# Kernel optimization log

Measured on AMD Instinct MI355X. Metric: run time of the kernel, lower is better.

Reference implementation:

```python
import jax, jax.numpy as jnp
import numpy as np

PS = 8  # window_size
LOCAL = 16  # split channels

def conv1x1(x, w, b):
    return jnp.einsum('oi,bihw->bohw', w, x) + b[None, :, None, None]

def dynamic_local(x, w1, b1, w2, b2, k):
    # x: (B, C, H, W); dynamic per-(batch,channel) depthwise conv with generated kernels
    B, C, H, W = x.shape
    pooled = x.mean((2, 3))                      # (B, C) adaptive avg pool to 1x1
    h = jax.nn.relu(pooled @ w1.T + b1)
    kern = (h @ w2.T + b2).reshape(B, C, k, k)   # per-sample depthwise kernels
    def per_batch(xb, kb):
        return jax.lax.conv_general_dilated(
            xb[None], kb[:, None], (1, 1), 'SAME',
            feature_group_count=C,
            dimension_numbers=('NCHW', 'OIHW', 'NCHW'))[0]
    return jax.vmap(per_batch)(x, kern)

def channel_layernorm(x, w, b, eps=1e-6):
    # LayerNorm over channel dim (torch module's non-channels_last path)
    u = x.mean(1, keepdims=True)
    s = ((x - u) ** 2).mean(1, keepdims=True)
    xn = (x - u) / jnp.sqrt(s + eps)
    return w[None, :, None, None] * xn + b[None, :, None, None]

def fsas(x, hid_w, hid_b, dw_w, dw_b, ln_w, ln_b, out_w, out_b):
    hidden = conv1x1(x, hid_w, hid_b)
    mid = hidden.shape[1]
    dw = jax.lax.conv_general_dilated(
        hidden, dw_w[:, None], (1, 1), 'SAME',
        feature_group_count=mid,
        dimension_numbers=('NCHW', 'OIHW', 'NCHW')) + dw_b[None, :, None, None]
    q, k, v = jnp.split(dw, 3, axis=1)
    B, C, H, W = q.shape
    def patch(t):
        # (B,C,H,W) -> (B,C,H/ps,W/ps,ps,ps)
        return t.reshape(B, C, H // PS, PS, W // PS, PS).transpose(0, 1, 2, 4, 3, 5)
    qf = jnp.fft.rfft2(patch(q))
    kf = jnp.fft.rfft2(patch(k))
    out = jnp.fft.irfft2(qf * kf, s=(PS, PS))
    out = out.transpose(0, 1, 2, 4, 3, 5).reshape(B, C, H, W)
    out = channel_layernorm(out, ln_w, ln_b)
    return conv1x1(v * out, out_w, out_b)


def setup_inputs() -> dict:
    key = jax.random.key(0)
    ks = jax.random.split(key, 12)
    s = 0.02
    return {
        'x': jax.random.normal(ks[0], (4, 64, 256, 256), jnp.float32),
        'dl1_w1': jax.random.normal(ks[1], (16, 16), jnp.float32) * s,
        'dl1_b1': jnp.zeros((16,), jnp.float32),
        'dl1_w2': jax.random.normal(ks[2], (144, 16), jnp.float32) * s,
        'dl1_b2': jnp.zeros((144,), jnp.float32),
        'dl2_w1': jax.random.normal(ks[3], (16, 16), jnp.float32) * s,
        'dl2_b1': jnp.zeros((16,), jnp.float32),
        'dl2_w2': jax.random.normal(ks[4], (400, 16), jnp.float32) * s,
        'dl2_b2': jnp.zeros((400,), jnp.float32),
        'fs_hid_w': jax.random.normal(ks[5], (144, 48), jnp.float32) * s,
        'fs_hid_b': jnp.zeros((144,), jnp.float32),
        'fs_dw_w': jax.random.normal(ks[6], (144, 3, 3), jnp.float32) * s,
        'fs_dw_b': jnp.zeros((144,), jnp.float32),
        'fs_ln_w': jnp.ones((48,), jnp.float32),
        'fs_ln_b': jnp.zeros((48,), jnp.float32),
        'fs_out_w': jax.random.normal(ks[7], (48, 48), jnp.float32) * s,
        'fs_out_b': jnp.zeros((48,), jnp.float32),
        'last_w': jax.random.normal(ks[8], (64, 64), jnp.float32) * s,
        'last_b': jnp.zeros((64,), jnp.float32),
    }


def reference(x, dl1_w1, dl1_b1, dl1_w2, dl1_b2, dl2_w1, dl2_b1, dl2_w2, dl2_b2,
              fs_hid_w, fs_hid_b, fs_dw_w, fs_dw_b, fs_ln_w, fs_ln_b,
              fs_out_w, fs_out_b, last_w, last_b):
    x1, x2 = x[:, :LOCAL], x[:, LOCAL:]
    x1 = dynamic_local(x1, dl1_w1, dl1_b1, dl1_w2, dl1_b2, 3)
    x1 = dynamic_local(x1, dl2_w1, dl2_b1, dl2_w2, dl2_b2, 5)
    x2 = fsas(x2, fs_hid_w, fs_hid_b, fs_dw_w, fs_dw_b, fs_ln_w, fs_ln_b, fs_out_w, fs_out_b)
    return conv1x1(jnp.concatenate([x1, x2], axis=1), last_w, last_b)
```

## Files before the change

### kernel.cpp

```cpp
#include <hip/hip_runtime.h>

typedef _Float16 h2 __attribute__((ext_vector_type(2)));
typedef _Float16 h4 __attribute__((ext_vector_type(4)));
typedef _Float16 h8 __attribute__((ext_vector_type(8)));
typedef float f4 __attribute__((ext_vector_type(4)));

#if defined(__has_builtin)
#if __has_builtin(__builtin_amdgcn_fdot2)
#define HAS_FDOT2 1
#endif
#endif

__device__ __forceinline__ float warpsum(float v) {
    for (int off = 32; off > 0; off >>= 1) v += __shfl_down(v, off);
    return v;
}

__device__ __forceinline__ int aswz(int p, int k) {
    return p * 72 + ((((k >> 3) ^ (p >> 3)) & 7) << 3) + (k & 7);
}
__device__ __forceinline__ int sswz(int p, int k) {
    return p * 64 + ((((k >> 3) ^ (p >> 3)) & 7) << 3) + (k & 7);
}

__global__ __launch_bounds__(256) void k_prep(const float* __restrict__ hid_w,
                                              const float* __restrict__ out_w,
                                              const float* __restrict__ last_w,
                                              _Float16* __restrict__ hwH,
                                              _Float16* __restrict__ owlwH) {
    int t = blockIdx.x * 256 + threadIdx.x;
    int stride = gridDim.x * 256;
    for (int i = t; i < 10368; i += stride) {
        int n = i / 72, k = i - n * 72;
        hwH[i] = (k < 48) ? (_Float16)hid_w[n * 48 + k] : (_Float16)0.f;
    }
    for (int i = t; i < 3456; i += stride) {
        int n = i / 72, k = i - n * 72;
        owlwH[i] = (k < 48) ? (_Float16)out_w[n * 48 + k] : (_Float16)0.f;
    }
    for (int i = t; i < 4608; i += stride) {
        int n = i / 72, k = i - n * 72;
        owlwH[3456 + i] = (k < 64) ? (_Float16)last_w[n * 64 + k] : (_Float16)0.f;
    }
}

__global__ __launch_bounds__(256) void k_pool(const float* __restrict__ x, float* __restrict__ pooled1) {
    int bid = blockIdx.x;
    int b = bid >> 4, c = bid & 15;
    const float* base = x + (size_t)(b * 64 + c) * 65536;
    float s = 0.f;
    for (int i = threadIdx.x; i < 16384; i += 256) {
        float4 v = ((const float4*)base)[i];
        s += v.x + v.y + v.z + v.w;
    }
    __shared__ float red[4];
    s = warpsum(s);
    if ((threadIdx.x & 63) == 0) red[threadIdx.x >> 6] = s;
    __syncthreads();
    if (threadIdx.x == 0) pooled1[bid] = (red[0] + red[1] + red[2] + red[3]) * (1.f / 65536.f);
}

__global__ __launch_bounds__(256) void k_kern1(const float* __restrict__ pooled1,
                                               const float* __restrict__ w1, const float* __restrict__ b1,
                                               const float* __restrict__ w2, const float* __restrict__ b2,
                                               float* __restrict__ kern1) {
    __shared__ float h[64];
    int t = threadIdx.x;
    if (t < 64) {
        int b = t >> 4, j = t & 15;
        float a = b1[j];
        for (int i = 0; i < 16; ++i) a += pooled1[b * 16 + i] * w1[j * 16 + i];
        h[t] = fmaxf(a, 0.f);
    }
    __syncthreads();
    for (int i = t; i < 576; i += 256) {
        int b = i / 144, o = i - b * 144;
        float a = b2[o];
        for (int j = 0; j < 16; ++j) a += h[b * 16 + j] * w2[o * 16 + j];
        kern1[i] = a;
    }
}

__global__ __launch_bounds__(256) void k_dw3(const float* __restrict__ x,
                                             const float* __restrict__ kern1,
                                             float* __restrict__ y1, float* __restrict__ rowsum) {
    __shared__ float tile[10][258];
    __shared__ float red[8][4];
    int bid = blockIdx.x;
    int rb = bid & 31, bc = bid >> 5;
    int b = bc >> 4, c = bc & 15;
    int row0 = rb << 3;
    int col = threadIdx.x;
    const float* xc = x + ((size_t)(b * 64 + c) << 16);
#pragma unroll
    for (int j = 0; j < 10; ++j) {
        int r = row0 - 1 + j;
        tile[j][col + 1] = ((unsigned)r < 256u) ? xc[(r << 8) + col] : 0.f;
    }
    if (col < 10) { tile[col][0] = 0.f; tile[col][257] = 0.f; }
    const float* k9 = kern1 + b * 144 + c * 9;
    float kk[9];
#pragma unroll
    for (int i = 0; i < 9; ++i) kk[i] = k9[i];
    __syncthreads();
#pragma unroll
    for (int j = 0; j < 8; ++j) {
        float acc = 0.f;
#pragma unroll
        for (int dy = 0; dy < 3; ++dy)
#pragma unroll
            for (int dx = 0; dx < 3; ++dx)
                acc += kk[dy * 3 + dx] * tile[j + dy][col + dx];
        y1[((size_t)bc << 16) + ((row0 + j) << 8) + col] = acc;
        float s = warpsum(acc);
        if ((col & 63) == 0) red[j][col >> 6] = s;
    }
    __syncthreads();
    if (col < 8) rowsum[bc * 256 + row0 + col] = red[col][0] + red[col][1] + red[col][2] + red[col][3];
}

__global__ __launch_bounds__(256) void k_kern2(const float* __restrict__ rowsum,
                                               const float* __restrict__ w1, const float* __restrict__ b1,
                                               const float* __restrict__ w2, const float* __restrict__ b2,
                                               float* __restrict__ kern2) {
    __shared__ float ps[256];
    __shared__ float p2[64];
    __shared__ float h[64];
    int t = threadIdx.x;
    {
        int pair = t >> 2, seg = t & 3;
        const float* rs = rowsum + pair * 256 + seg * 64;
        float s = 0.f;
        for (int j = 0; j < 64; ++j) s += rs[j];
        ps[t] = s;
    }
    __syncthreads();
    if (t < 64) p2[t] = (ps[t * 4] + ps[t * 4 + 1] + ps[t * 4 + 2] + ps[t * 4 + 3]) * (1.f / 65536.f);
    __syncthreads();
    if (t < 64) {
        int b = t >> 4, j = t & 15;
        float a = b1[j];
        for (int i = 0; i < 16; ++i) a += p2[b * 16 + i] * w1[j * 16 + i];
        h[t] = fmaxf(a, 0.f);
    }
    __syncthreads();
    for (int i = t; i < 1600; i += 256) {
        int b = i / 400, o = i - b * 400;
        float a = b2[o];
        for (int j = 0; j < 16; ++j) a += h[b * 16 + j] * w2[o * 16 + j];
        kern2[i] = a;
    }
}

__global__ __launch_bounds__(256) void k_dw5(const float* __restrict__ y1,
                                             const float* __restrict__ kern2,
                                             float* __restrict__ x1o) {
    __shared__ float tile[12][260];
    int bid = blockIdx.x;
    int rb = bid & 31, bc = bid >> 5;
    int b = bc >> 4, c = bc & 15;
    int row0 = rb << 3;
    int col = threadIdx.x;
    const float* yc = y1 + ((size_t)bc << 16);
#pragma unroll
    for (int j = 0; j < 12; ++j) {
        int r = row0 - 2 + j;
        tile[j][col + 2] = ((unsigned)r < 256u) ? yc[(r << 8) + col] : 0.f;
    }
    if (col < 12) { tile[col][0] = 0.f; tile[col][1] = 0.f; tile[col][258] = 0.f; tile[col][259] = 0.f; }
    const float* k25 = kern2 + b * 400 + c * 25;
    float kk[25];
#pragma unroll
    for (int i = 0; i < 25; ++i) kk[i] = k25[i];
    __syncthreads();
#pragma unroll
    for (int j = 0; j < 8; ++j) {
        float acc = 0.f;
#pragma unroll
        for (int dy = 0; dy < 5; ++dy)
#pragma unroll
            for (int dx = 0; dx < 5; ++dx)
                acc += kk[dy * 5 + dx] * tile[j + dy][col + dx];
        x1o[((size_t)bc << 16) + ((row0 + j) << 8) + col] = acc;
    }
}

__global__ __launch_bounds__(512, 4) void k_fsas(const float* __restrict__ x,
                                                 const _Float16* __restrict__ hwH, const float* __restrict__ hid_b,
                                                 const float* __restrict__ dw_w, const float* __restrict__ dw_b,
                                                 const float* __restrict__ ln_w, const float* __restrict__ ln_b,
                                                 const _Float16* __restrict__ owlwH, const float* __restrict__ out_b,
                                                 const float* __restrict__ last_b,
                                                 const float* __restrict__ x1o, float* __restrict__ out) {
    __shared__ __align__(16) _Float16 Sbig[17856];
    __shared__ __align__(16) _Float16 vbuf[3456];
    __shared__ __align__(16) _Float16 qbuf[3072];
    __shared__ __align__(16) _Float16 kbuf2[6528];
    __shared__ __align__(16) float pstat[128];

    _Float16* Abuf  = Sbig;
    _Float16* hbuf  = Sbig;
    _Float16* fbuf  = Sbig;
    float*    lnp   = (float*)(Sbig + 4608);
    _Float16* outb  = Sbig + 6656;
    _Float16* sbufA = kbuf2;

    int tid = threadIdx.x;
    int lane = tid & 63;
    int wave = __builtin_amdgcn_readfirstlane(tid >> 6);
    int bid = blockIdx.x;
    int swz = ((bid & 7) << 9) | (bid >> 3);
    int b = swz >> 10;
    int rem = swz & 1023;
    int row0 = (rem >> 5) << 3, col0 = (rem & 31) << 3;

    int l16 = lane & 15, lhi = lane >> 4;
    int mb = wave * 16 + (lhi << 2);
    bool st[4], vok[4];
#pragma unroll
    for (int r = 0; r < 4; ++r) {
        int m = mb + r;
        st[r] = (m < 120);
        int yv = m / 12, xv = m - yv * 12;
        vok[r] = st[r] && (xv < 10) &&
                 ((unsigned)(row0 - 1 + yv) < 256u) && ((unsigned)(col0 - 1 + xv) < 256u);
    }

    h8 wb0[9], wb1[9];
    float biasr[9];
#pragma unroll
    for (int nt = 0; nt < 9; ++nt) {
        const _Float16* wr = hwH + (nt * 16 + l16) * 72 + (lhi << 3);
        wb0[nt] = *(const h8*)(wr);
        wb1[nt] = *(const h8*)(wr + 32);
        biasr[nt] = hid_b[nt * 16 + l16];
    }
    float xr[8];
    int fpx = lane, fgrp = wave - 6;
    if (wave >= 6) {
        size_t gp = ((size_t)(row0 + (fpx >> 3)) << 8) + col0 + (fpx & 7);
#pragma unroll
        for (int j = 0; j < 8; ++j)
            xr[j] = x1o[((size_t)(b * 16 + fgrp * 8 + j) << 16) + gp];
    }

    if (tid < 480) {
        int k = tid / 10, y = tid - (tid / 10) * 10;
        int gy = row0 - 1 + y;
        bool rowok = (unsigned)gy < 256u;
        const float* xk = x + ((size_t)(b * 64 + 16 + k) << 16) + ((size_t)(gy & 255) << 8);
#pragma unroll
        for (int xx = 0; xx < 10; ++xx) {
            int gx = col0 - 1 + xx;
            float v = (rowok && (unsigned)gx < 256u) ? xk[gx] : 0.f;
            Abuf[aswz(y * 12 + xx, k)] = (_Float16)v;
        }
        Abuf[aswz(y * 12 + 10, k)] = (_Float16)0.f;
        Abuf[aswz(y * 12 + 11, k)] = (_Float16)0.f;
    }
    if (tid < 256) {
        int p = tid >> 1, kb = 48 + ((tid & 1) << 3);
        *(h8*)(Abuf + aswz(p, kb)) = (h8)(_Float16)0.f;
    }
    if (tid < 48) {
        int p = 120 + tid / 6, kb = (tid % 6) << 3;
        *(h8*)(Abuf + aswz(p, kb)) = (h8)(_Float16)0.f;
    }
    __syncthreads();

    int arow = wave * 16 + l16;
    h8 a0 = *(const h8*)(Abuf + aswz(arow, lhi << 3));
    h8 a1 = *(const h8*)(Abuf + aswz(arow, 32 + (lhi << 3)));
    __syncthreads();

#pragma unroll
    for (int nt = 0; nt < 9; ++nt) {
        float bias = biasr[nt];
        f4 acc = {bias, bias, bias, bias};
        acc = __builtin_amdgcn_mfma_f32_16x16x32_f16(a0, wb0[nt], acc, 0, 0, 0);
        acc = __builtin_amdgcn_mfma_f32_16x16x32_f16(a1, wb1[nt], acc, 0, 0, 0);
        int n_l = nt * 16 + l16;
#pragma unroll
        for (int r = 0; r < 4; ++r)
            if (st[r]) hbuf[n_l * 124 + mb + r] = vok[r] ? (_Float16)acc[r] : (_Float16)0.f;
    }
    __syncthreads();

    {
        int row = tid & 7;
        auto dw_task = [&](int ch) {
            const float* dwp = dw_w + ch * 9;
            float o[8];
            float bias = dw_b[ch];
#pragma unroll
            for (int xx = 0; xx < 8; ++xx) o[xx] = bias;
            const _Float16* hb = hbuf + ch * 124 + row * 12;
#pragma unroll
            for (int dy = 0; dy < 3; ++dy) {
                h4 r0 = *(const h4*)(hb + dy * 12);
                h4 r1 = *(const h4*)(hb + dy * 12 + 4);
                h2 r2 = *(const h2*)(hb + dy * 12 + 8);
                float rowv[10] = {(float)r0[0], (float)r0[1], (float)r0[2], (float)r0[3],
                                  (float)r1[0], (float)r1[1], (float)r1[2], (float)r1[3],
                                  (float)r2[0], (float)r2[1]};
                float w0 = dwp[dy * 3], w1 = dwp[dy * 3 + 1], w2 = dwp[dy * 3 + 2];
#pragma unroll
                for (int xx = 0; xx < 8; ++xx)
                    o[xx] += w0 * rowv[xx] + w1 * rowv[xx + 1] + w2 * rowv[xx + 2];
            }
            if (ch < 48) {
                h8 qv;
#pragma unroll
                for (int xx = 0; xx < 8; ++xx) qv[xx] = (_Float16)o[xx];
                *(h8*)(qbuf + ch * 64 + row * 8) = qv;
            } else if (ch < 96) {
                int kc = ch - 48;
                h8 kr, ko;
#pragma unroll
                for (int t2 = 0; t2 < 8; ++t2) {
                    kr[t2] = (_Float16)o[(8 - t2) & 7];
                    ko[t2] = (_Float16)o[(9 - t2) & 7];
                }
                *(h8*)(kbuf2 + kc * 136 + row * 16) = kr;
                *(h8*)(kbuf2 + kc * 136 + row * 16 + 8) = ko;
            } else {
                int vc = ch - 96;
                h8 vv;
#pragma unroll
                for (int xx = 0; xx < 8; ++xx) vv[xx] = (_Float16)o[xx];
                *(h8*)(vbuf + vc * 72 + row * 8) = vv;
            }
        };
        dw_task(tid >> 3);
        dw_task(64 + (tid >> 3));
        if (tid < 128) dw_task(128 + (tid >> 3));
    }
    __syncthreads();

    float co[8];
    int dch = tid >> 3, drow = tid & 7;
    if (tid < 384) {
        int ch = dch, m = drow;
#pragma unroll
        for (int n = 0; n < 8; ++n) co[n] = 0.f;
#pragma unroll
        for (int i8 = 0; i8 < 8; ++i8) {
            int r = (m - i8) & 7;
            h8 q8 = *(const h8*)(qbuf + ch * 64 + i8 * 8);
            h8 e8 = *(const h8*)(kbuf2 + ch * 136 + r * 16);
#ifdef HAS_FDOT2
            h8 o8 = *(const h8*)(kbuf2 + ch * 136 + r * 16 + 8);
            h2 qp[4], ep[4], op[4];
            qp[0] = __builtin_shufflevector(q8, q8, 0, 1); qp[1] = __builtin_shufflevector(q8, q8, 2, 3);
            qp[2] = __builtin_shufflevector(q8, q8, 4, 5); qp[3] = __builtin_shufflevector(q8, q8, 6, 7);
            ep[0] = __builtin_shufflevector(e8, e8, 0, 1); ep[1] = __builtin_shufflevector(e8, e8, 2, 3);
            ep[2] = __builtin_shufflevector(e8, e8, 4, 5); ep[3] = __builtin_shufflevector(e8, e8, 6, 7);
            op[0] = __builtin_shufflevector(o8, o8, 0, 1); op[1] = __builtin_shufflevector(o8, o8, 2, 3);
            op[2] = __builtin_shufflevector(o8, o8, 4, 5); op[3] = __builtin_shufflevector(o8, o8, 6, 7);
#pragma unroll
            for (int u = 0; u < 4; ++u)
#pragma unroll
                for (int a = 0; a < 4; ++a) {
                    co[2 * u]     = __builtin_amdgcn_fdot2(qp[a], ep[(a - u) & 3], co[2 * u], false);
                    co[2 * u + 1] = __builtin_amdgcn_fdot2(qp[a], op[(a - u) & 3], co[2 * u + 1], false);
                }
#else
            float qf[8], kf[8];
#pragma unroll
            for (int j = 0; j < 8; ++j) { qf[j] = (float)q8[j]; kf[j] = (float)e8[(8 - j) & 7]; }
#pragma unroll
            for (int j = 0; j < 8; ++j)
#pragma unroll
                for (int n = 0; n < 8; ++n)
                    co[n] += qf[j] * kf[(n - j) & 7];
#endif
        }
#pragma unroll
        for (int v = 0; v < 4; ++v)
            *(h2*)(outb + dch * 66 + drow * 8 + 2 * v) = (h2){(_Float16)co[2 * v], (_Float16)co[2 * v + 1]};
    } else {
        h8 fv;
#pragma unroll
        for (int j = 0; j < 8; ++j) fv[j] = (_Float16)xr[j];
        *(h8*)(fbuf + aswz(fpx, fgrp * 8)) = fv;
    }
    __syncthreads();

    {
        int px = tid & 63, g = tid >> 6;
        float s = 0.f, ss = 0.f;
#pragma unroll
        for (int cc = 0; cc < 6; ++cc) {
            float v = (float)outb[(g * 6 + cc) * 66 + px];
            s += v; ss += v * v;
        }
        lnp[g * 64 + px] = s;
        lnp[512 + g * 64 + px] = ss;
    }
    __syncthreads();
    if (tid < 64) {
        float s = 0.f, ss = 0.f;
#pragma unroll
        for (int g = 0; g < 8; ++g) { s += lnp[g * 64 + tid]; ss += lnp[512 + g * 64 + tid]; }
        float mu = s * (1.f / 48.f);
        float var = ss * (1.f / 48.f) - mu * mu;
        pstat[tid * 2] = mu;
        pstat[tid * 2 + 1] = rsqrtf(var + 1e-6f);
    }
    __syncthreads();

    if (tid < 384) {
        int ch = dch, m = drow;
        float lw = ln_w[ch], lb = ln_b[ch];
        h8 vv = *(const h8*)(vbuf + ch * 72 + m * 8);
        const float* ps = pstat + m * 16;
#pragma unroll
        for (int n = 0; n < 8; ++n) {
            float mu = ps[2 * n], inv = ps[2 * n + 1];
            float lnv = lw * ((co[n] - mu) * inv) + lb;
            sbufA[sswz(m * 8 + n, ch)] = (_Float16)((float)vv[n] * lnv);
        }
    }
    *(h2*)(sbufA + sswz(lane, 48 + (wave << 1))) = (h2){(_Float16)0.f, (_Float16)0.f};
    __syncthreads();

    for (int t = wave; t < 12; t += 8) {
        int mt = t / 3, nt = t - mt * 3;
        int row5 = mt * 16 + l16;
        h8 c0 = *(const h8*)(sbufA + sswz(row5, lhi << 3));
        h8 c1 = *(const h8*)(sbufA + sswz(row5, 32 + (lhi << 3)));
        h8 d0 = *(const h8*)(owlwH + nt * 1152 + l16 * 72 + (lhi << 3));
        h8 d1 = *(const h8*)(owlwH + nt * 1152 + l16 * 72 + 32 + (lhi << 3));
        float bias = out_b[nt * 16 + l16];
        f4 acc = {bias, bias, bias, bias};
        acc = __builtin_amdgcn_mfma_f32_16x16x32_f16(c0, d0, acc, 0, 0, 0);
        acc = __builtin_amdgcn_mfma_f32_16x16x32_f16(c1, d1, acc, 0, 0, 0);
        int n5 = nt * 16 + l16;
        int pb = mt * 16 + (lhi << 2);
#pragma unroll
        for (int r = 0; r < 4; ++r)
            fbuf[aswz(pb + r, 16 + n5)] = (_Float16)acc[r];
    }
    __syncthreads();

    for (int t = wave; t < 16; t += 8) {
        int mt = t >> 2, nt = t & 3;
        int row6 = mt * 16 + l16;
        h8 c0 = *(const h8*)(fbuf + aswz(row6, lhi << 3));
        h8 c1 = *(const h8*)(fbuf + aswz(row6, 32 + (lhi << 3)));
        h8 d0 = *(const h8*)(owlwH + 3456 + nt * 1152 + l16 * 72 + (lhi << 3));
        h8 d1 = *(const h8*)(owlwH + 3456 + nt * 1152 + l16 * 72 + 32 + (lhi << 3));
        float bias = last_b[nt * 16 + l16];
        f4 acc = {bias, bias, bias, bias};
        acc = __builtin_amdgcn_mfma_f32_16x16x32_f16(c0, d0, acc, 0, 0, 0);
        acc = __builtin_amdgcn_mfma_f32_16x16x32_f16(c1, d1, acc, 0, 0, 0);
        int ch = nt * 16 + l16;
        int px0 = mt * 16 + (lhi << 2);
        float4 val = {acc[0], acc[1], acc[2], acc[3]};
        *(float4*)(out + ((size_t)(b * 64 + ch) << 16) + ((size_t)(row0 + (px0 >> 3)) << 8) + col0 + (px0 & 7)) = val;
    }
}

extern "C" void kernel_launch(void* const* d_in, const int* in_sizes, int n_in,
                              void* d_out, int out_size, void* d_ws, size_t ws_size,
                              hipStream_t stream) {
    const float* x      = (const float*)d_in[0];
    const float* dl1_w1 = (const float*)d_in[1];
    const float* dl1_b1 = (const float*)d_in[2];
    const float* dl1_w2 = (const float*)d_in[3];
    const float* dl1_b2 = (const float*)d_in[4];
    const float* dl2_w1 = (const float*)d_in[5];
    const float* dl2_b1 = (const float*)d_in[6];
    const float* dl2_w2 = (const float*)d_in[7];
    const float* dl2_b2 = (const float*)d_in[8];
    const float* hid_w  = (const float*)d_in[9];
    const float* hid_b  = (const float*)d_in[10];
    const float* dw_w   = (const float*)d_in[11];
    const float* dw_b   = (const float*)d_in[12];
    const float* ln_w   = (const float*)d_in[13];
    const float* ln_b   = (const float*)d_in[14];
    const float* out_w  = (const float*)d_in[15];
    const float* out_b  = (const float*)d_in[16];
    const float* last_w = (const float*)d_in[17];
    const float* last_b = (const float*)d_in[18];
    float* out = (float*)d_out;

    float* ws      = (float*)d_ws;
    float* pooled1 = ws;
    float* kern1   = ws + 64;
    float* rowsum  = ws + 1024;
    float* kern2   = ws + 17408;
    _Float16* hwH   = (_Float16*)(ws + 19008);
    _Float16* owlwH = (_Float16*)(ws + 24192);
    float* y1      = ws + 32768;
    float* x1o     = ws + 32768 + 4194304;

    k_prep <<<8,    256, 0, stream>>>(hid_w, out_w, last_w, hwH, owlwH);
    k_pool <<<64,   256, 0, stream>>>(x, pooled1);
    k_kern1<<<1,    256, 0, stream>>>(pooled1, dl1_w1, dl1_b1, dl1_w2, dl1_b2, kern1);
    k_dw3  <<<2048, 256, 0, stream>>>(x, kern1, y1, rowsum);
    k_kern2<<<1,    256, 0, stream>>>(rowsum, dl2_w1, dl2_b1, dl2_w2, dl2_b2, kern2);
    k_dw5  <<<2048, 256, 0, stream>>>(y1, kern2, x1o);
    k_fsas <<<4096, 512, 0, stream>>>(x, hwH, hid_b, dw_w, dw_b, ln_w, ln_b,
                                      owlwH, out_b, last_b, x1o, out);
}
```

Measured before the change: 167.1 us.

## Shrink LDS and registers in fused FSAS kernel to raise occupancy

The fused FSAS kernel drops the separate v buffer and keeps v in registers. The doubled k buffer is replaced by an alignbit-derived odd-shift view, so q and k share one smaller LDS array that is reused as the staging buffer. Hidden-projection weights are now loaded per tile instead of held in registers, and launch bounds go from 4 to 6 waves per SIMD. The depthwise 3x3 now uses packed fp16 fdot2 with fp16 weights, the input load packs two channels per store, and the XOR swizzle on the A/f buffers is removed. Risks are extra fp16 rounding in the depthwise conv, possible LDS bank conflicts without the swizzle, and register spills under the tighter bound.

New measurement: 167.2 us. About the same (+0.1%).

```diff
diff --git a/kernel.cpp b/kernel.cpp
--- a/kernel.cpp
+++ b/kernel.cpp
@@ -4,21 +4,17 @@
 typedef _Float16 h4 __attribute__((ext_vector_type(4)));
 typedef _Float16 h8 __attribute__((ext_vector_type(8)));
 typedef float f4 __attribute__((ext_vector_type(4)));
-
-#if defined(__has_builtin)
-#if __has_builtin(__builtin_amdgcn_fdot2)
-#define HAS_FDOT2 1
-#endif
-#endif
+typedef unsigned int u32;
+typedef u32 u32x2 __attribute__((ext_vector_type(2)));
+typedef u32 u32x4 __attribute__((ext_vector_type(4)));
+
+__device__ __forceinline__ h2 bch2(u32 v) { return __builtin_bit_cast(h2, v); }
 
 __device__ __forceinline__ float warpsum(float v) {
     for (int off = 32; off > 0; off >>= 1) v += __shfl_down(v, off);
     return v;
 }
 
-__device__ __forceinline__ int aswz(int p, int k) {
-    return p * 72 + ((((k >> 3) ^ (p >> 3)) & 7) << 3) + (k & 7);
-}
 __device__ __forceinline__ int sswz(int p, int k) {
     return p * 64 + ((((k >> 3) ^ (p >> 3)) & 7) << 3) + (k & 7);
 }
@@ -185,7 +181,7 @@
     }
 }
 
-__global__ __launch_bounds__(512, 4) void k_fsas(const float* __restrict__ x,
+__global__ __launch_bounds__(512, 6) void k_fsas(const float* __restrict__ x,
                                                  const _Float16* __restrict__ hwH, const float* __restrict__ hid_b,
                                                  const float* __restrict__ dw_w, const float* __restrict__ dw_b,
                                                  const float* __restrict__ ln_w, const float* __restrict__ ln_b,
@@ -193,9 +189,7 @@
                                                  const float* __restrict__ last_b,
                                                  const float* __restrict__ x1o, float* __restrict__ out) {
     __shared__ __align__(16) _Float16 Sbig[17856];
-    __shared__ __align__(16) _Float16 vbuf[3456];
-    __shared__ __align__(16) _Float16 qbuf[3072];
-    __shared__ __align__(16) _Float16 kbuf2[6528];
+    __shared__ __align__(16) _Float16 qk[6144];
     __shared__ __align__(16) float pstat[128];
 
     _Float16* Abuf  = Sbig;
@@ -203,7 +197,9 @@
     _Float16* fbuf  = Sbig;
     float*    lnp   = (float*)(Sbig + 4608);
     _Float16* outb  = Sbig + 6656;
-    _Float16* sbufA = kbuf2;
+    _Float16* qbuf  = qk;
+    _Float16* kbuf  = qk + 3072;
+    _Float16* sbufA = qk;
 
     int tid = threadIdx.x;
     int lane = tid & 63;
@@ -216,25 +212,43 @@
 
     int l16 = lane & 15, lhi = lane >> 4;
     int mb = wave * 16 + (lhi << 2);
-    bool st[4], vok[4];
+    bool vok[4];
 #pragma unroll
     for (int r = 0; r < 4; ++r) {
         int m = mb + r;
-        st[r] = (m < 120);
         int yv = m / 12, xv = m - yv * 12;
-        vok[r] = st[r] && (xv < 10) &&
+        vok[r] = (m < 120) && (xv < 10) &&
                  ((unsigned)(row0 - 1 + yv) < 256u) && ((unsigned)(col0 - 1 + xv) < 256u);
     }
 
-    h8 wb0[9], wb1[9];
-    float biasr[9];
-#pragma unroll
-    for (int nt = 0; nt < 9; ++nt) {
-        const _Float16* wr = hwH + (nt * 16 + l16) * 72 + (lhi << 3);
-        wb0[nt] = *(const h8*)(wr);
-        wb1[nt] = *(const h8*)(wr + 32);
-        biasr[nt] = hid_b[nt * 16 + l16];
-    }
+    if (tid < 480) {
+        int k2 = tid / 20, r20 = tid - (tid / 20) * 20;
+        int y = r20 >> 1, xh = r20 & 1;
+        int gy = row0 - 1 + y;
+        bool rowok = (unsigned)gy < 256u;
+        const float* xa = x + ((size_t)(b * 64 + 16 + 2 * k2) << 16) + ((size_t)(gy & 255) << 8);
+        const float* xb = xa + 65536;
+#pragma unroll
+        for (int xx = 0; xx < 6; ++xx) {
+            int xv = xh * 6 + xx;
+            int gx = col0 - 1 + xv;
+            bool ok = rowok && (xv < 10) && ((unsigned)gx < 256u);
+            float va = ok ? xa[gx] : 0.f;
+            float vb = ok ? xb[gx] : 0.f;
+            *(h2*)(Abuf + (y * 12 + xv) * 72 + 2 * k2) = (h2){(_Float16)va, (_Float16)vb};
+        }
+    }
+    if (tid < 240) {
+        int p = tid >> 1, kb = 48 + ((tid & 1) << 3);
+        *(h8*)(Abuf + p * 72 + kb) = (h8)(_Float16)0.f;
+    }
+    __syncthreads();
+
+    int arow = wave * 16 + l16;
+    h8 a0 = *(const h8*)(Abuf + arow * 72 + (lhi << 3));
+    h8 a1 = *(const h8*)(Abuf + arow * 72 + 32 + (lhi << 3));
+    __syncthreads();
+
     float xr[8];
     int fpx = lane, fgrp = wave - 6;
     if (wave >= 6) {
@@ -244,101 +258,93 @@
             xr[j] = x1o[((size_t)(b * 16 + fgrp * 8 + j) << 16) + gp];
     }
 
-    if (tid < 480) {
-        int k = tid / 10, y = tid - (tid / 10) * 10;
-        int gy = row0 - 1 + y;
-        bool rowok = (unsigned)gy < 256u;
-        const float* xk = x + ((size_t)(b * 64 + 16 + k) << 16) + ((size_t)(gy & 255) << 8);
-#pragma unroll
-        for (int xx = 0; xx < 10; ++xx) {
-            int gx = col0 - 1 + xx;
-            float v = (rowok && (unsigned)gx < 256u) ? xk[gx] : 0.f;
-            Abuf[aswz(y * 12 + xx, k)] = (_Float16)v;
-        }
-        Abuf[aswz(y * 12 + 10, k)] = (_Float16)0.f;
-        Abuf[aswz(y * 12 + 11, k)] = (_Float16)0.f;
-    }
-    if (tid < 256) {
-        int p = tid >> 1, kb = 48 + ((tid & 1) << 3);
-        *(h8*)(Abuf + aswz(p, kb)) = (h8)(_Float16)0.f;
-    }
-    if (tid < 48) {
-        int p = 120 + tid / 6, kb = (tid % 6) << 3;
-        *(h8*)(Abuf + aswz(p, kb)) = (h8)(_Float16)0.f;
-    }
-    __syncthreads();
-
-    int arow = wave * 16 + l16;
-    h8 a0 = *(const h8*)(Abuf + aswz(arow, lhi << 3));
-    h8 a1 = *(const h8*)(Abuf + aswz(arow, 32 + (lhi << 3)));
-    __syncthreads();
-
 #pragma unroll
     for (int nt = 0; nt < 9; ++nt) {
-        float bias = biasr[nt];
+        const _Float16* wr = hwH + (nt * 16 + l16) * 72 + (lhi << 3);
+        h8 b0 = *(const h8*)(wr);
+        h8 b1 = *(const h8*)(wr + 32);
+        float bias = hid_b[nt * 16 + l16];
         f4 acc = {bias, bias, bias, bias};
-        acc = __builtin_amdgcn_mfma_f32_16x16x32_f16(a0, wb0[nt], acc, 0, 0, 0);
-        acc = __builtin_amdgcn_mfma_f32_16x16x32_f16(a1, wb1[nt], acc, 0, 0, 0);
+        acc = __builtin_amdgcn_mfma_f32_16x16x32_f16(a0, b0, acc, 0, 0, 0);
+        acc = __builtin_amdgcn_mfma_f32_16x16x32_f16(a1, b1, acc, 0, 0, 0);
         int n_l = nt * 16 + l16;
-#pragma unroll
-        for (int r = 0; r < 4; ++r)
-            if (st[r]) hbuf[n_l * 124 + mb + r] = vok[r] ? (_Float16)acc[r] : (_Float16)0.f;
-    }
-    __syncthreads();
-
-    {
-        int row = tid & 7;
-        auto dw_task = [&](int ch) {
-            const float* dwp = dw_w + ch * 9;
-            float o[8];
-            float bias = dw_b[ch];
-#pragma unroll
-            for (int xx = 0; xx < 8; ++xx) o[xx] = bias;
-            const _Float16* hb = hbuf + ch * 124 + row * 12;
-#pragma unroll
-            for (int dy = 0; dy < 3; ++dy) {
-                h4 r0 = *(const h4*)(hb + dy * 12);
-                h4 r1 = *(const h4*)(hb + dy * 12 + 4);
-                h2 r2 = *(const h2*)(hb + dy * 12 + 8);
-                float rowv[10] = {(float)r0[0], (float)r0[1], (float)r0[2], (float)r0[3],
-                                  (float)r1[0], (float)r1[1], (float)r1[2], (float)r1[3],
-                                  (float)r2[0], (float)r2[1]};
-                float w0 = dwp[dy * 3], w1 = dwp[dy * 3 + 1], w2 = dwp[dy * 3 + 2];
-#pragma unroll
-                for (int xx = 0; xx < 8; ++xx)
-                    o[xx] += w0 * rowv[xx] + w1 * rowv[xx + 1] + w2 * rowv[xx + 2];
-            }
-            if (ch < 48) {
-                h8 qv;
-#pragma unroll
-                for (int xx = 0; xx < 8; ++xx) qv[xx] = (_Float16)o[xx];
-                *(h8*)(qbuf + ch * 64 + row * 8) = qv;
-            } else if (ch < 96) {
-                int kc = ch - 48;
-                h8 kr, ko;
-#pragma unroll
-                for (int t2 = 0; t2 < 8; ++t2) {
-                    kr[t2] = (_Float16)o[(8 - t2) & 7];
-                    ko[t2] = (_Float16)o[(9 - t2) & 7];
-                }
-                *(h8*)(kbuf2 + kc * 136 + row * 16) = kr;
-                *(h8*)(kbuf2 + kc * 136 + row * 16 + 8) = ko;
-            } else {
-                int vc = ch - 96;
-                h8 vv;
-#pragma unroll
-                for (int xx = 0; xx < 8; ++xx) vv[xx] = (_Float16)o[xx];
-                *(h8*)(vbuf + vc * 72 + row * 8) = vv;
-            }
-        };
-        dw_task(tid >> 3);
-        dw_task(64 + (tid >> 3));
-        if (tid < 128) dw_task(128 + (tid >> 3));
+        if (mb < 120) {
+            h2 p0 = {vok[0] ? (_Float16)acc[0] : (_Float16)0.f, vok[1] ? (_Float16)acc[1] : (_Float16)0.f};
+            h2 p1 = {vok[2] ? (_Float16)acc[2] : (_Float16)0.f, vok[3] ? (_Float16)acc[3] : (_Float16)0.f};
+            *(h2*)(hbuf + n_l * 124 + mb) = p0;
+            *(h2*)(hbuf + n_l * 124 + mb + 2) = p1;
+        }
+    }
+    __syncthreads();
+
+    int dch = tid >> 3, drow = tid & 7;
+    h8 vreg;
+    auto dw_row = [&](int ch, int row, float o[8]) {
+        const float* dwp = dw_w + ch * 9;
+        float bias = dw_b[ch];
+#pragma unroll
+        for (int xx = 0; xx < 8; ++xx) o[xx] = bias;
+        const _Float16* hb = hbuf + ch * 124 + row * 12;
+#pragma unroll
+        for (int dy = 0; dy < 3; ++dy) {
+            u32x2 A2 = *(const u32x2*)(hb + dy * 12);
+            u32x2 B2 = *(const u32x2*)(hb + dy * 12 + 4);
+            u32 r89 = *(const u32*)(hb + dy * 12 + 8);
+            u32 r01 = A2.x, r23 = A2.y, r45 = B2.x, r67 = B2.y;
+            u32 s12 = __builtin_amdgcn_alignbit(r23, r01, 16);
+            u32 s34 = __builtin_amdgcn_alignbit(r45, r23, 16);
+            u32 s56 = __builtin_amdgcn_alignbit(r67, r45, 16);
+            u32 s78 = __builtin_amdgcn_alignbit(r89, r67, 16);
+            _Float16 w0 = (_Float16)dwp[dy * 3], w1 = (_Float16)dwp[dy * 3 + 1], w2 = (_Float16)dwp[dy * 3 + 2];
+            h2 w01 = {w0, w1};
+            h2 w2lo = {w2, (_Float16)0.f};
+            h2 w2hi = {(_Float16)0.f, w2};
+            o[0] = __builtin_amdgcn_fdot2(w01, bch2(r01), o[0], false);
+            o[0] = __builtin_amdgcn_fdot2(w2lo, bch2(r23), o[0], false);
+            o[1] = __builtin_amdgcn_fdot2(w01, bch2(s12), o[1], false);
+            o[1] = __builtin_amdgcn_fdot2(w2lo, bch2(s34), o[1], false);
+            o[2] = __builtin_amdgcn_fdot2(w01, bch2(r23), o[2], false);
+            o[2] = __builtin_amdgcn_fdot2(w2lo, bch2(r45), o[2], false);
+            o[3] = __builtin_amdgcn_fdot2(w01, bch2(s34), o[3], false);
+            o[3] = __builtin_amdgcn_fdot2(w2lo, bch2(s56), o[3], false);
+            o[4] = __builtin_amdgcn_fdot2(w01, bch2(r45), o[4], false);
+            o[4] = __builtin_amdgcn_fdot2(w2lo, bch2(r67), o[4], false);
+            o[5] = __builtin_amdgcn_fdot2(w01, bch2(s56), o[5], false);
+            o[5] = __builtin_amdgcn_fdot2(w2lo, bch2(s78), o[5], false);
+            o[6] = __builtin_amdgcn_fdot2(w01, bch2(r67), o[6], false);
+            o[6] = __builtin_amdgcn_fdot2(w2lo, bch2(r89), o[6], false);
+            o[7] = __builtin_amdgcn_fdot2(w01, bch2(s78), o[7], false);
+            o[7] = __builtin_amdgcn_fdot2(w2hi, bch2(r89), o[7], false);
+        }
+    };
+    if (tid < 384) {
+        float oq[8];
+        dw_row(dch, drow, oq);
+        h8 qv;
+#pragma unroll
+        for (int xx = 0; xx < 8; ++xx) qv[xx] = (_Float16)oq[xx];
+        *(h8*)(qbuf + dch * 64 + drow * 8) = qv;
+        float ov[8];
+        dw_row(96 + dch, drow, ov);
+#pragma unroll
+        for (int xx = 0; xx < 8; ++xx) vreg[xx] = (_Float16)ov[xx];
+    } else {
+        int j0 = (tid - 384) * 3;
+#pragma unroll
+        for (int i = 0; i < 3; ++i) {
+            int j = j0 + i;
+            int kc = j >> 3, kr = j & 7;
+            float ok8[8];
+            dw_row(48 + kc, kr, ok8);
+            h8 krv;
+#pragma unroll
+            for (int t2 = 0; t2 < 8; ++t2) krv[t2] = (_Float16)ok8[(8 - t2) & 7];
+            *(h8*)(kbuf + kc * 64 + kr * 8) = krv;
+        }
     }
     __syncthreads();
 
     float co[8];
-    int dch = tid >> 3, drow = tid & 7;
     if (tid < 384) {
         int ch = dch, m = drow;
 #pragma unroll
@@ -346,17 +352,14 @@
 #pragma unroll
         for (int i8 = 0; i8 < 8; ++i8) {
             int r = (m - i8) & 7;
-            h8 q8 = *(const h8*)(qbuf + ch * 64 + i8 * 8);
-            h8 e8 = *(const h8*)(kbuf2 + ch * 136 + r * 16);
-#ifdef HAS_FDOT2
-            h8 o8 = *(const h8*)(kbuf2 + ch * 136 + r * 16 + 8);
-            h2 qp[4], ep[4], op[4];
-            qp[0] = __builtin_shufflevector(q8, q8, 0, 1); qp[1] = __builtin_shufflevector(q8, q8, 2, 3);
-            qp[2] = __builtin_shufflevector(q8, q8, 4, 5); qp[3] = __builtin_shufflevector(q8, q8, 6, 7);
-            ep[0] = __builtin_shufflevector(e8, e8, 0, 1); ep[1] = __builtin_shufflevector(e8, e8, 2, 3);
-            ep[2] = __builtin_shufflevector(e8, e8, 4, 5); ep[3] = __builtin_shufflevector(e8, e8, 6, 7);
-            op[0] = __builtin_shufflevector(o8, o8, 0, 1); op[1] = __builtin_shufflevector(o8, o8, 2, 3);
-            op[2] = __builtin_shufflevector(o8, o8, 4, 5); op[3] = __builtin_shufflevector(o8, o8, 6, 7);
+            u32x4 qv = *(const u32x4*)(qbuf + ch * 64 + i8 * 8);
+            u32x4 ev = *(const u32x4*)(kbuf + ch * 64 + r * 8);
+            h2 qp[4] = {bch2(qv.x), bch2(qv.y), bch2(qv.z), bch2(qv.w)};
+            h2 ep[4] = {bch2(ev.x), bch2(ev.y), bch2(ev.z), bch2(ev.w)};
+            h2 op[4] = {bch2(__builtin_amdgcn_alignbit(ev.x, ev.w, 16)),
+                        bch2(__builtin_amdgcn_alignbit(ev.y, ev.x, 16)),
+                        bch2(__builtin_amdgcn_alignbit(ev.z, ev.y, 16)),
+                        bch2(__builtin_amdgcn_alignbit(ev.w, ev.z, 16))};
 #pragma unroll
             for (int u = 0; u < 4; ++u)
 #pragma unroll
@@ -364,16 +367,6 @@
                     co[2 * u]     = __builtin_amdgcn_fdot2(qp[a], ep[(a - u) & 3], co[2 * u], false);
                     co[2 * u + 1] = __builtin_amdgcn_fdot2(qp[a], op[(a - u) & 3], co[2 * u + 1], false);
                 }
-#else
-            float qf[8], kf[8];
-#pragma unroll
-            for (int j = 0; j < 8; ++j) { qf[j] = (float)q8[j]; kf[j] = (float)e8[(8 - j) & 7]; }
-#pragma unroll
-            for (int j = 0; j < 8; ++j)
-#pragma unroll
-                for (int n = 0; n < 8; ++n)
-                    co[n] += qf[j] * kf[(n - j) & 7];
-#endif
         }
 #pragma unroll
         for (int v = 0; v < 4; ++v)
@@ -382,7 +375,7 @@
         h8 fv;
 #pragma unroll
         for (int j = 0; j < 8; ++j) fv[j] = (_Float16)xr[j];
-        *(h8*)(fbuf + aswz(fpx, fgrp * 8)) = fv;
+        *(h8*)(fbuf + fpx * 72 + fgrp * 8) = fv;
     }
     __syncthreads();
 
@@ -410,15 +403,13 @@
     __syncthreads();
 
     if (tid < 384) {
-        int ch = dch, m = drow;
-        float lw = ln_w[ch], lb = ln_b[ch];
-        h8 vv = *(const h8*)(vbuf + ch * 72 + m * 8);
-        const float* ps = pstat + m * 16;
+        float lw = ln_w[dch], lb = ln_b[dch];
+        const float* ps = pstat + drow * 16;
 #pragma unroll
         for (int n = 0; n < 8; ++n) {
             float mu = ps[2 * n], inv = ps[2 * n + 1];
             float lnv = lw * ((co[n] - mu) * inv) + lb;
-            sbufA[sswz(m * 8 + n, ch)] = (_Float16)((float)vv[n] * lnv);
+            sbufA[sswz(drow * 8 + n, dch)] = (_Float16)((float)vreg[n] * lnv);
         }
     }
     *(h2*)(sbufA + sswz(lane, 48 + (wave << 1))) = (h2){(_Float16)0.f, (_Float16)0.f};
@@ -439,15 +430,15 @@
         int pb = mt * 16 + (lhi << 2);
 #pragma unroll
         for (int r = 0; r < 4; ++r)
-            fbuf[aswz(pb + r, 16 + n5)] = (_Float16)acc[r];
+            fbuf[(pb + r) * 72 + 16 + n5] = (_Float16)acc[r];
     }
     __syncthreads();
 
     for (int t = wave; t < 16; t += 8) {
         int mt = t >> 2, nt = t & 3;
         int row6 = mt * 16 + l16;
-        h8 c0 = *(const h8*)(fbuf + aswz(row6, lhi << 3));
-        h8 c1 = *(const h8*)(fbuf + aswz(row6, 32 + (lhi << 3)));
+        h8 c0 = *(const h8*)(fbuf + row6 * 72 + (lhi << 3));
+        h8 c1 = *(const h8*)(fbuf + row6 * 72 + 32 + (lhi << 3));
         h8 d0 = *(const h8*)(owlwH + 3456 + nt * 1152 + l16 * 72 + (lhi << 3));
         h8 d1 = *(const h8*)(owlwH + 3456 + nt * 1152 + l16 * 72 + 32 + (lhi << 3));
         float bias = last_b[nt * 16 + l16];
```
